# Kernel tuning notes

Hardware: AMD Instinct MI355X
Metric: run time of the kernel (lower is better)

Reference implementation:

```python
import jax, jax.numpy as jnp
import numpy as np

NUM_EMBEDDINGS = 8192
EMBEDDING_DIM = 256
PROJECTION_DIM = 128


def setup_inputs() -> dict:
    key = jax.random.key(0)
    k_x, k_cb, k_w, k_b = jax.random.split(key, 4)
    x = jax.random.normal(k_x, (16, 1024, EMBEDDING_DIM), dtype=jnp.float32)
    codebook = jax.random.normal(k_cb, (NUM_EMBEDDINGS, EMBEDDING_DIM), dtype=jnp.float32)
    proj_w = jax.random.normal(k_w, (EMBEDDING_DIM, PROJECTION_DIM), dtype=jnp.float32) / np.sqrt(EMBEDDING_DIM)
    proj_b = jax.random.normal(k_b, (PROJECTION_DIM,), dtype=jnp.float32) * 0.01
    return {"x": x, "codebook": codebook, "proj_w": proj_w, "proj_b": proj_b}


def reference(x, codebook, proj_w, proj_b):
    # Flatten tokens: [N, D]
    x_flat = x.reshape(-1, EMBEDDING_DIM)
    # Project tokens and codebook into the distance space: [N, P], [K, P]
    x_proj = x_flat @ proj_w + proj_b
    cb_proj = codebook @ proj_w + proj_b
    # Squared euclidean distances via expansion: [N, K]
    distances = (
        jnp.sum(x_proj ** 2, axis=1, keepdims=True)
        - 2.0 * (x_proj @ cb_proj.T)
        + jnp.sum(cb_proj ** 2, axis=1)
    )
    idx = jnp.argmin(distances, axis=1)
    discrete = jax.nn.one_hot(idx, NUM_EMBEDDINGS, dtype=x.dtype)  # [N, K]
    # One-hot matmul lookup (disguised gather): [N, D]
    quantized = (discrete @ codebook).reshape(x.shape)
    return (discrete, quantized)
```

## Files before the change

### kernel.cpp

```cpp
#include <hip/hip_runtime.h>
#include <math.h>

#define D 256
#define P 128
#define K 8192
#define NTOK 16384
#define NROWS (NTOK + K)
#define NCHUNK 8
#define KCHUNK (K / NCHUNK)
#define CAP 15
#define MARGIN 3.0f
#define FLT_BIG 3.402823466e+38f

typedef __attribute__((ext_vector_type(8))) short bf16x8;
typedef __attribute__((ext_vector_type(4))) float f32x4;
typedef __attribute__((ext_vector_type(8))) unsigned short u16x8;

__device__ __forceinline__ unsigned short f32_to_bf16_rne(float f) {
    unsigned int u = __float_as_uint(f);
    u = (u + 0x7fffu + ((u >> 16) & 1u)) >> 16;
    return (unsigned short)u;
}

__global__ __launch_bounds__(256) void proj_kernel(
    const float* __restrict__ x, const float* __restrict__ cb,
    const float* __restrict__ w, const float* __restrict__ bias,
    float* __restrict__ xproj, float* __restrict__ cproj,
    float* __restrict__ xnorm, float* __restrict__ cnorm,
    unsigned short* __restrict__ xh, unsigned short* __restrict__ ch)
{
    __shared__ float As[16][D];
    const int tid = threadIdx.x;
    const int row0 = blockIdx.x * 16;

    for (int i = tid; i < 16 * (D / 4); i += 256) {
        int r = i / (D / 4);
        int c4 = i % (D / 4);
        int gr = row0 + r;
        const float* src = (gr < NTOK) ? (x + (size_t)gr * D)
                                       : (cb + (size_t)(gr - NTOK) * D);
        float4 v = ((const float4*)src)[c4];
        ((float4*)&As[r][0])[c4] = v;
    }
    __syncthreads();

    const int r = tid >> 4;
    const int c0 = (tid & 15) * 8;

    float acc[8];
#pragma unroll
    for (int j = 0; j < 8; j++) acc[j] = 0.f;

    for (int d = 0; d < D; d += 4) {
        float4 a4 = *(const float4*)&As[r][d];
#pragma unroll
        for (int dd = 0; dd < 4; dd++) {
            float av = (dd == 0) ? a4.x : (dd == 1) ? a4.y : (dd == 2) ? a4.z : a4.w;
            float4 w0 = *(const float4*)&w[(size_t)(d + dd) * P + c0];
            float4 w1 = *(const float4*)&w[(size_t)(d + dd) * P + c0 + 4];
            acc[0] = fmaf(av, w0.x, acc[0]);
            acc[1] = fmaf(av, w0.y, acc[1]);
            acc[2] = fmaf(av, w0.z, acc[2]);
            acc[3] = fmaf(av, w0.w, acc[3]);
            acc[4] = fmaf(av, w1.x, acc[4]);
            acc[5] = fmaf(av, w1.y, acc[5]);
            acc[6] = fmaf(av, w1.z, acc[6]);
            acc[7] = fmaf(av, w1.w, acc[7]);
        }
    }

    float out[8];
    float nrm = 0.f;
    u16x8 hv;
#pragma unroll
    for (int j = 0; j < 8; j++) {
        out[j] = acc[j] + bias[c0 + j];
        nrm = fmaf(out[j], out[j], nrm);
        hv[j] = f32_to_bf16_rne(out[j]);
    }

    const int gr = row0 + r;
    float* dst;
    unsigned short* hdst;
    if (gr < NTOK) { dst = xproj + (size_t)gr * P; hdst = xh + (size_t)gr * P; }
    else           { dst = cproj + (size_t)(gr - NTOK) * P; hdst = ch + (size_t)(gr - NTOK) * P; }
    float4 o0; o0.x = out[0]; o0.y = out[1]; o0.z = out[2]; o0.w = out[3];
    float4 o1; o1.x = out[4]; o1.y = out[5]; o1.z = out[6]; o1.w = out[7];
    *(float4*)&dst[c0] = o0;
    *(float4*)&dst[c0 + 4] = o1;
    *(u16x8*)&hdst[c0] = hv;

#pragma unroll
    for (int off = 1; off < 16; off <<= 1)
        nrm += __shfl_xor(nrm, off, 16);
    if ((tid & 15) == 0) {
        if (gr < NTOK) xnorm[gr] = nrm;
        else           cnorm[gr - NTOK] = nrm;
    }
}

__global__ __launch_bounds__(256) void filter_kernel(
    const unsigned short* __restrict__ xh, const unsigned short* __restrict__ ch,
    const float* __restrict__ xnorm, const float* __restrict__ cnorm,
    float* __restrict__ chunkmin, int* __restrict__ cand)
{
    __shared__ short sa[64][136];
    __shared__ short sb[64][136];
    __shared__ float smin[64];
    __shared__ int scnt[64];
    __shared__ int scand[64][CAP];

    const int tid = threadIdx.x;
    const int tok0 = blockIdx.x * 64;
    const int chunk = blockIdx.y;
    const int k0 = chunk * KCHUNK;

    const int wave = tid >> 6;
    const int lane = tid & 63;
    const int quad = lane >> 4;
    const int l15 = lane & 15;
    const int wm = wave >> 1;
    const int wn = wave & 1;

    for (int i = tid; i < 64 * 16; i += 256) {
        int row = i >> 4;
        int c8 = i & 15;
        uint4 v = *(const uint4*)(xh + (size_t)(tok0 + row) * P + c8 * 8);
        *(uint4*)&sa[row][c8 * 8] = v;
    }
    if (tid < 64) { smin[tid] = FLT_BIG; scnt[tid] = 0; }

    float xnv[2][4];
#pragma unroll
    for (int mi = 0; mi < 2; mi++)
#pragma unroll
        for (int r = 0; r < 4; r++)
            xnv[mi][r] = xnorm[tok0 + wm * 32 + mi * 16 + quad * 4 + r];

    for (int ct = 0; ct < KCHUNK / 64; ct++) {
        const int kt = k0 + ct * 64;
        __syncthreads();
        for (int i = tid; i < 64 * 16; i += 256) {
            int row = i >> 4;
            int c8 = i & 15;
            uint4 v = *(const uint4*)(ch + (size_t)(kt + row) * P + c8 * 8);
            *(uint4*)&sb[row][c8 * 8] = v;
        }
        __syncthreads();

        f32x4 acc[2][2];
#pragma unroll
        for (int mi = 0; mi < 2; mi++)
#pragma unroll
            for (int nj = 0; nj < 2; nj++)
                acc[mi][nj] = (f32x4)(0.f);

#pragma unroll
        for (int ks = 0; ks < 4; ks++) {
            const int kf = ks * 32 + quad * 8;
            bf16x8 a0 = *(const bf16x8*)&sa[wm * 32 + l15][kf];
            bf16x8 a1 = *(const bf16x8*)&sa[wm * 32 + 16 + l15][kf];
            bf16x8 b0 = *(const bf16x8*)&sb[wn * 32 + l15][kf];
            bf16x8 b1 = *(const bf16x8*)&sb[wn * 32 + 16 + l15][kf];
            acc[0][0] = __builtin_amdgcn_mfma_f32_16x16x32_bf16(a0, b0, acc[0][0], 0, 0, 0);
            acc[0][1] = __builtin_amdgcn_mfma_f32_16x16x32_bf16(a0, b1, acc[0][1], 0, 0, 0);
            acc[1][0] = __builtin_amdgcn_mfma_f32_16x16x32_bf16(a1, b0, acc[1][0], 0, 0, 0);
            acc[1][1] = __builtin_amdgcn_mfma_f32_16x16x32_bf16(a1, b1, acc[1][1], 0, 0, 0);
        }

        float cn0 = cnorm[kt + wn * 32 + l15];
        float cn1 = cnorm[kt + wn * 32 + 16 + l15];
        float d[2][2][4];
        float mn[2][4];
#pragma unroll
        for (int mi = 0; mi < 2; mi++)
#pragma unroll
            for (int r = 0; r < 4; r++) {
                float d0 = (xnv[mi][r] - 2.0f * acc[mi][0][r]) + cn0;
                float d1 = (xnv[mi][r] - 2.0f * acc[mi][1][r]) + cn1;
                d[mi][0][r] = d0;
                d[mi][1][r] = d1;
                mn[mi][r] = fminf(d0, d1);
            }
#pragma unroll
        for (int off = 1; off < 16; off <<= 1) {
#pragma unroll
            for (int mi = 0; mi < 2; mi++)
#pragma unroll
                for (int r = 0; r < 4; r++)
                    mn[mi][r] = fminf(mn[mi][r], __shfl_xor(mn[mi][r], off));
        }
        if (l15 == 0) {
#pragma unroll
            for (int mi = 0; mi < 2; mi++)
#pragma unroll
                for (int r = 0; r < 4; r++) {
                    int tl = wm * 32 + mi * 16 + quad * 4 + r;
                    atomicMin((int*)&smin[tl], __float_as_int(mn[mi][r]));
                }
        }
        __syncthreads();

#pragma unroll
        for (int mi = 0; mi < 2; mi++)
#pragma unroll
            for (int r = 0; r < 4; r++) {
                int tl = wm * 32 + mi * 16 + quad * 4 + r;
                float thr = smin[tl] + MARGIN;
#pragma unroll
                for (int nj = 0; nj < 2; nj++) {
                    if (d[mi][nj][r] <= thr) {
                        int pos = atomicAdd(&scnt[tl], 1);
                        if (pos < CAP)
                            scand[tl][pos] = kt + wn * 32 + nj * 16 + l15;
                    }
                }
            }
    }
    __syncthreads();

    if (tid < 64) {
        int t = tok0 + tid;
        int cnt = scnt[tid];
        if (cnt > CAP) cnt = CAP;
        int* rec = cand + ((size_t)t * NCHUNK + chunk) * (CAP + 1);
        rec[0] = cnt;
        for (int j = 0; j < cnt; j++) rec[1 + j] = scand[tid][j];
        chunkmin[(size_t)t * NCHUNK + chunk] = smin[tid];
    }
}

__global__ __launch_bounds__(256) void rescore_kernel(
    const float* __restrict__ xproj, const float* __restrict__ cproj,
    const float* __restrict__ xnorm, const float* __restrict__ cnorm,
    const float* __restrict__ chunkmin, const int* __restrict__ cand,
    int* __restrict__ fidx)
{
    const int tid = threadIdx.x;
    const int lane = tid & 63;
    const int wave = tid >> 6;
    const int t = blockIdx.x * 4 + wave;

    float cm = (lane < NCHUNK) ? chunkmin[(size_t)t * NCHUNK + lane] : FLT_BIG;
#pragma unroll
    for (int off = 1; off < 8; off <<= 1)
        cm = fminf(cm, __shfl_xor(cm, off));
    float mg = __shfl(cm, 0);

    const float xn = xnorm[t];
    float bv = FLT_BIG;
    int bi = 0x7fffffff;

    for (int c = 0; c < NCHUNK; c++) {
        if (chunkmin[(size_t)t * NCHUNK + c] > mg + MARGIN) continue;
        const int* rec = cand + ((size_t)t * NCHUNK + c) * (CAP + 1);
        int cnt = rec[0];
        for (int j = 0; j < cnt; j++) {
            if (((c * CAP + j) & 63) != lane) continue;
            int k = rec[1 + j];
            const float* xr = xproj + (size_t)t * P;
            const float* cr = cproj + (size_t)k * P;
            float s = 0.f;
            for (int p = 0; p < P; p += 4) {
                float4 a = *(const float4*)&xr[p];
                float4 b = *(const float4*)&cr[p];
                s = fmaf(a.x, b.x, s);
                s = fmaf(a.y, b.y, s);
                s = fmaf(a.z, b.z, s);
                s = fmaf(a.w, b.w, s);
            }
            float dist = (xn - 2.0f * s) + cnorm[k];
            if (dist < bv || (dist == bv && k < bi)) { bv = dist; bi = k; }
        }
    }

#pragma unroll
    for (int off = 1; off < 64; off <<= 1) {
        float ov = __shfl_xor(bv, off);
        int oi = __shfl_xor(bi, off);
        if (ov < bv || (ov == bv && oi < bi)) { bv = ov; bi = oi; }
    }
    if (lane == 0) fidx[t] = bi;
}

__global__ __launch_bounds__(256) void output_kernel(
    const int* __restrict__ fidx, const float* __restrict__ cb,
    float* __restrict__ discrete, float* __restrict__ quant)
{
    __shared__ int sidx[8];
    const int tid = threadIdx.x;
    const int tok0 = blockIdx.x * 8;
    if (tid < 8) sidx[tid] = fidx[tok0 + tid];
    __syncthreads();

    for (int i = tid; i < 8 * (K / 4); i += 256) {
        int tl = i >> 11;
        int f4 = i & 2047;
        int id = sidx[tl];
        f32x4 v = (f32x4)(0.f);
        if (f4 == (id >> 2)) v[id & 3] = 1.f;
        __builtin_nontemporal_store(v, (f32x4*)(discrete + (size_t)(tok0 + tl) * K + f4 * 4));
    }

    for (int i = tid; i < 8 * (D / 4); i += 256) {
        int tl = i >> 6;
        int c4 = i & 63;
        float4 v = ((const float4*)(cb + (size_t)sidx[tl] * D))[c4];
        ((float4*)(quant + (size_t)(tok0 + tl) * D))[c4] = v;
    }
}

extern "C" void kernel_launch(void* const* d_in, const int* in_sizes, int n_in,
                              void* d_out, int out_size, void* d_ws, size_t ws_size,
                              hipStream_t stream) {
    const float* x    = (const float*)d_in[0];
    const float* cb   = (const float*)d_in[1];
    const float* w    = (const float*)d_in[2];
    const float* bias = (const float*)d_in[3];

    float* out = (float*)d_out;
    float* discrete = out;
    float* quant = out + (size_t)NTOK * K;

    char* ws = (char*)d_ws;
    size_t off = 0;
    float* xproj = (float*)(ws + off); off += (size_t)NTOK * P * 4;
    float* cproj = (float*)(ws + off); off += (size_t)K * P * 4;
    float* xnorm = (float*)(ws + off); off += (size_t)NTOK * 4;
    float* cnorm = (float*)(ws + off); off += (size_t)K * 4;
    unsigned short* xh = (unsigned short*)(ws + off); off += (size_t)NTOK * P * 2;
    unsigned short* ch = (unsigned short*)(ws + off); off += (size_t)K * P * 2;
    float* chunkmin = (float*)(ws + off); off += (size_t)NTOK * NCHUNK * 4;
    int* cand = (int*)(ws + off); off += (size_t)NTOK * NCHUNK * (CAP + 1) * 4;
    int* fidx = (int*)(ws + off); off += (size_t)NTOK * 4;

    proj_kernel<<<dim3(NROWS / 16), dim3(256), 0, stream>>>(
        x, cb, w, bias, xproj, cproj, xnorm, cnorm, xh, ch);

    filter_kernel<<<dim3(NTOK / 64, NCHUNK), dim3(256), 0, stream>>>(
        xh, ch, xnorm, cnorm, chunkmin, cand);

    rescore_kernel<<<dim3(NTOK / 4), dim3(256), 0, stream>>>(
        xproj, cproj, xnorm, cnorm, chunkmin, cand, fidx);

    output_kernel<<<dim3(NTOK / 8), dim3(256), 0, stream>>>(
        fidx, cb, discrete, quant);
}
```

Baseline: 996.5 us.

## Keep token fragments in registers and give each wave whole codebook tile

The filter kernel now gives each block 128 tokens instead of 64. Each wave holds its 32-token A fragments in registers for the whole chunk instead of staging them in shared memory, and computes all 64 codebook columns of every tile, so one codebook tile load serves twice as many tokens. The per-row minimum is now a running minimum kept per wave, which removes the shared atomicMin and one barrier per tile. In exchange, more accumulators and A fragments raise register pressure, and there are half as many blocks.

```diff
diff --git a/kernel.cpp b/kernel.cpp
--- a/kernel.cpp
+++ b/kernel.cpp
@@ -104,14 +104,13 @@
     const float* __restrict__ xnorm, const float* __restrict__ cnorm,
     float* __restrict__ chunkmin, int* __restrict__ cand)
 {
-    __shared__ short sa[64][136];
     __shared__ short sb[64][136];
-    __shared__ float smin[64];
-    __shared__ int scnt[64];
-    __shared__ int scand[64][CAP];
+    __shared__ float smin[128];
+    __shared__ int scnt[128];
+    __shared__ int scand[128][CAP];
 
     const int tid = threadIdx.x;
-    const int tok0 = blockIdx.x * 64;
+    const int tok0 = blockIdx.x * 128;
     const int chunk = blockIdx.y;
     const int k0 = chunk * KCHUNK;
 
@@ -119,23 +118,29 @@
     const int lane = tid & 63;
     const int quad = lane >> 4;
     const int l15 = lane & 15;
-    const int wm = wave >> 1;
-    const int wn = wave & 1;
-
-    for (int i = tid; i < 64 * 16; i += 256) {
-        int row = i >> 4;
-        int c8 = i & 15;
-        uint4 v = *(const uint4*)(xh + (size_t)(tok0 + row) * P + c8 * 8);
-        *(uint4*)&sa[row][c8 * 8] = v;
-    }
-    if (tid < 64) { smin[tid] = FLT_BIG; scnt[tid] = 0; }
+
+    if (tid < 128) scnt[tid] = 0;
+
+    bf16x8 afrag[2][4];
+#pragma unroll
+    for (int mi = 0; mi < 2; mi++)
+#pragma unroll
+        for (int ks = 0; ks < 4; ks++)
+            afrag[mi][ks] = *(const bf16x8*)(
+                xh + (size_t)(tok0 + wave * 32 + mi * 16 + l15) * P + ks * 32 + quad * 8);
 
     float xnv[2][4];
 #pragma unroll
     for (int mi = 0; mi < 2; mi++)
 #pragma unroll
         for (int r = 0; r < 4; r++)
-            xnv[mi][r] = xnorm[tok0 + wm * 32 + mi * 16 + quad * 4 + r];
+            xnv[mi][r] = xnorm[tok0 + wave * 32 + mi * 16 + quad * 4 + r];
+
+    float rmin[2][4];
+#pragma unroll
+    for (int mi = 0; mi < 2; mi++)
+#pragma unroll
+        for (int r = 0; r < 4; r++) rmin[mi][r] = FLT_BIG;
 
     for (int ct = 0; ct < KCHUNK / 64; ct++) {
         const int kt = k0 + ct * 64;
@@ -148,78 +153,71 @@
         }
         __syncthreads();
 
-        f32x4 acc[2][2];
+        f32x4 acc[2][4];
 #pragma unroll
         for (int mi = 0; mi < 2; mi++)
 #pragma unroll
-            for (int nj = 0; nj < 2; nj++)
+            for (int nj = 0; nj < 4; nj++)
                 acc[mi][nj] = (f32x4)(0.f);
 
 #pragma unroll
         for (int ks = 0; ks < 4; ks++) {
             const int kf = ks * 32 + quad * 8;
-            bf16x8 a0 = *(const bf16x8*)&sa[wm * 32 + l15][kf];
-            bf16x8 a1 = *(const bf16x8*)&sa[wm * 32 + 16 + l15][kf];
-            bf16x8 b0 = *(const bf16x8*)&sb[wn * 32 + l15][kf];
-            bf16x8 b1 = *(const bf16x8*)&sb[wn * 32 + 16 + l15][kf];
-            acc[0][0] = __builtin_amdgcn_mfma_f32_16x16x32_bf16(a0, b0, acc[0][0], 0, 0, 0);
-            acc[0][1] = __builtin_amdgcn_mfma_f32_16x16x32_bf16(a0, b1, acc[0][1], 0, 0, 0);
-            acc[1][0] = __builtin_amdgcn_mfma_f32_16x16x32_bf16(a1, b0, acc[1][0], 0, 0, 0);
-            acc[1][1] = __builtin_amdgcn_mfma_f32_16x16x32_bf16(a1, b1, acc[1][1], 0, 0, 0);
+            bf16x8 b0 = *(const bf16x8*)&sb[l15][kf];
+            bf16x8 b1 = *(const bf16x8*)&sb[16 + l15][kf];
+            bf16x8 b2 = *(const bf16x8*)&sb[32 + l15][kf];
+            bf16x8 b3 = *(const bf16x8*)&sb[48 + l15][kf];
+            acc[0][0] = __builtin_amdgcn_mfma_f32_16x16x32_bf16(afrag[0][ks], b0, acc[0][0], 0, 0, 0);
+            acc[0][1] = __builtin_amdgcn_mfma_f32_16x16x32_bf16(afrag[0][ks], b1, acc[0][1], 0, 0, 0);
+            acc[0][2] = __builtin_amdgcn_mfma_f32_16x16x32_bf16(afrag[0][ks], b2, acc[0][2], 0, 0, 0);
+            acc[0][3] = __builtin_amdgcn_mfma_f32_16x16x32_bf16(afrag[0][ks], b3, acc[0][3], 0, 0, 0);
+            acc[1][0] = __builtin_amdgcn_mfma_f32_16x16x32_bf16(afrag[1][ks], b0, acc[1][0], 0, 0, 0);
+            acc[1][1] = __builtin_amdgcn_mfma_f32_16x16x32_bf16(afrag[1][ks], b1, acc[1][1], 0, 0, 0);
+            acc[1][2] = __builtin_amdgcn_mfma_f32_16x16x32_bf16(afrag[1][ks], b2, acc[1][2], 0, 0, 0);
+            acc[1][3] = __builtin_amdgcn_mfma_f32_16x16x32_bf16(afrag[1][ks], b3, acc[1][3], 0, 0, 0);
         }
 
-        float cn0 = cnorm[kt + wn * 32 + l15];
-        float cn1 = cnorm[kt + wn * 32 + 16 + l15];
-        float d[2][2][4];
-        float mn[2][4];
+        float cn[4];
+#pragma unroll
+        for (int nj = 0; nj < 4; nj++) cn[nj] = cnorm[kt + nj * 16 + l15];
+
 #pragma unroll
         for (int mi = 0; mi < 2; mi++)
 #pragma unroll
             for (int r = 0; r < 4; r++) {
-                float d0 = (xnv[mi][r] - 2.0f * acc[mi][0][r]) + cn0;
-                float d1 = (xnv[mi][r] - 2.0f * acc[mi][1][r]) + cn1;
-                d[mi][0][r] = d0;
-                d[mi][1][r] = d1;
-                mn[mi][r] = fminf(d0, d1);
-            }
-#pragma unroll
-        for (int off = 1; off < 16; off <<= 1) {
-#pragma unroll
-            for (int mi = 0; mi < 2; mi++)
-#pragma unroll
-                for (int r = 0; r < 4; r++)
-                    mn[mi][r] = fminf(mn[mi][r], __shfl_xor(mn[mi][r], off));
-        }
-        if (l15 == 0) {
-#pragma unroll
-            for (int mi = 0; mi < 2; mi++)
-#pragma unroll
-                for (int r = 0; r < 4; r++) {
-                    int tl = wm * 32 + mi * 16 + quad * 4 + r;
-                    atomicMin((int*)&smin[tl], __float_as_int(mn[mi][r]));
-                }
-        }
-        __syncthreads();
-
-#pragma unroll
-        for (int mi = 0; mi < 2; mi++)
-#pragma unroll
-            for (int r = 0; r < 4; r++) {
-                int tl = wm * 32 + mi * 16 + quad * 4 + r;
-                float thr = smin[tl] + MARGIN;
-#pragma unroll
-                for (int nj = 0; nj < 2; nj++) {
-                    if (d[mi][nj][r] <= thr) {
+                float d[4];
+#pragma unroll
+                for (int nj = 0; nj < 4; nj++)
+                    d[nj] = (xnv[mi][r] - 2.0f * acc[mi][nj][r]) + cn[nj];
+                float m = fminf(fminf(d[0], d[1]), fminf(d[2], d[3]));
+#pragma unroll
+                for (int off = 1; off < 16; off <<= 1)
+                    m = fminf(m, __shfl_xor(m, off));
+                float rm = fminf(rmin[mi][r], m);
+                rmin[mi][r] = rm;
+                float thr = rm + MARGIN;
+                int tl = wave * 32 + mi * 16 + quad * 4 + r;
+#pragma unroll
+                for (int nj = 0; nj < 4; nj++) {
+                    if (d[nj] <= thr) {
                         int pos = atomicAdd(&scnt[tl], 1);
                         if (pos < CAP)
-                            scand[tl][pos] = kt + wn * 32 + nj * 16 + l15;
+                            scand[tl][pos] = kt + nj * 16 + l15;
                     }
                 }
             }
     }
+
+    if (l15 == 0) {
+#pragma unroll
+        for (int mi = 0; mi < 2; mi++)
+#pragma unroll
+            for (int r = 0; r < 4; r++)
+                smin[wave * 32 + mi * 16 + quad * 4 + r] = rmin[mi][r];
+    }
     __syncthreads();
 
-    if (tid < 64) {
+    if (tid < 128) {
         int t = tok0 + tid;
         int cnt = scnt[tid];
         if (cnt > CAP) cnt = CAP;
@@ -337,7 +335,7 @@
     proj_kernel<<<dim3(NROWS / 16), dim3(256), 0, stream>>>(
         x, cb, w, bias, xproj, cproj, xnorm, cnorm, xh, ch);
 
-    filter_kernel<<<dim3(NTOK / 64, NCHUNK), dim3(256), 0, stream>>>(
+    filter_kernel<<<dim3(NTOK / 128, NCHUNK), dim3(256), 0, stream>>>(
         xh, ch, xnorm, cnorm, chunkmin, cand);
 
     rescore_kernel<<<dim3(NTOK / 4), dim3(256), 0, stream>>>(
```

After: 999.1 us. About the same (+0.3%).
